# Performance work log

Measured on AMD Instinct MI355X. Metric: run time of the kernel, lower is better.

## Reference

```python
import jax, jax.numpy as jnp
import numpy as np

BN_EPS = 1e-5

def _ste_sign(x):
    # forward: sign in {-1,+1}; backward: clipped straight-through (grad 1 on [-1,1])
    s = jnp.where(x >= 0, 1.0, -1.0).astype(x.dtype)
    c = jnp.clip(x, -1.0, 1.0)
    return c + jax.lax.stop_gradient(s - c)

def setup_inputs() -> dict:
    key = jax.random.key(0)
    ks = jax.random.split(key, 8)
    N, C, H, W = 32, 256, 56, 56
    x = jax.random.normal(ks[0], (N, C, H, W), dtype=jnp.float32)
    bias0 = jax.random.normal(ks[1], (C,), dtype=jnp.float32) * 0.1
    w = jax.random.normal(ks[2], (C, C, 1, 1), dtype=jnp.float32) * 0.05
    gamma = jnp.ones((C,), dtype=jnp.float32)
    beta = jnp.zeros((C,), dtype=jnp.float32)
    bias1 = jax.random.normal(ks[3], (C,), dtype=jnp.float32) * 0.1
    alpha = jnp.full((C,), 0.25, dtype=jnp.float32)  # PReLU init
    bias2 = jax.random.normal(ks[4], (C,), dtype=jnp.float32) * 0.1
    return {"x": x, "bias0": bias0, "w": w, "gamma": gamma, "beta": beta,
            "bias1": bias1, "alpha": alpha, "bias2": bias2}

def reference(x, bias0, w, gamma, beta, bias1, alpha, bias2):
    ch = lambda v: v[None, :, None, None]
    # move0: learnable per-channel bias
    out = x + ch(bias0)
    # binary activation: sign (STE)
    out = _ste_sign(out)
    # binarized 1x1 conv: w_bin = mean(|w|) per out-channel * sign(w)
    scale = jnp.mean(jnp.abs(w), axis=(1, 2, 3))              # [O]
    wb = scale[:, None] * _ste_sign(w[:, :, 0, 0])            # [O, C]
    out = jnp.einsum('nchw,oc->nohw', out, wb)                # 1x1 conv
    # bn1: batch statistics (training-mode math)
    mu = jnp.mean(out, axis=(0, 2, 3), keepdims=True)
    var = jnp.var(out, axis=(0, 2, 3), keepdims=True)
    out = ch(gamma) * (out - mu) * jax.lax.rsqrt(var + BN_EPS) + ch(beta)
    # residual add (downsample is None)
    out = out + x
    # move1 -> PReLU -> move2
    out = out + ch(bias1)
    out = jnp.where(out > 0, out, ch(alpha) * out)
    out = out + ch(bias2)
    return out
```

## Files before the change

kernel.cpp:

```cpp
#include <hip/hip_runtime.h>
#include <stdint.h>

typedef unsigned long long u64;
typedef unsigned int u32;

constexpr int kC  = 256;
constexpr int kHW = 3136;
constexpr int kN  = 32;
constexpr int kP  = kN * kHW;
constexpr int kPos = 64;
constexpr int kBlk = kP / kPos;
constexpr int kRedBlk  = 16;
constexpr int kRedRows = kBlk / kRedBlk;

constexpr size_t OFF_T     = 0;
constexpr size_t OFF_SCALE = 8192;
constexpr size_t OFF_SUMD  = 9216;
constexpr size_t OFF_SUMD2 = 11264;
constexpr size_t OFF_S     = 13312;
constexpr size_t OFF_PS    = 3224576;
constexpr size_t OFF_PQ    = 4830208;

struct alignas(16) U64x2 { u64 x, y; };

__global__ __launch_bounds__(256) void prep_kernel(
    const float* __restrict__ w, char* __restrict__ ws) {
  int t = threadIdx.x;
  int b = blockIdx.x;
  u64*   T     = (u64*)(ws + OFF_T);
  float* scale = (float*)(ws + OFF_SCALE);
  int kk = t >> 6, ln = t & 63;
  if (b == 0) {
    ((u64*)(ws + OFF_SUMD))[t]  = 0ull;
    ((u64*)(ws + OFF_SUMD2))[t] = 0ull;
  }
  __shared__ float part[4][16];
#pragma unroll
  for (int i = 0; i < 16; ++i) {
    int o = b * 16 + i;
    float v = w[o * kC + kk * 64 + ln];
    u64 m = __ballot(v >= 0.0f);
    float a = fabsf(v);
#pragma unroll
    for (int s = 32; s > 0; s >>= 1) a += __shfl_xor(a, s, 64);
    if (ln == 0) { T[kk * 256 + o] = m; part[kk][i] = a; }
  }
  __syncthreads();
  if (t < 16) {
    int o = b * 16 + t;
    scale[o] = (part[0][t] + part[1][t] + part[2][t] + part[3][t]) * (1.0f / 256.0f);
  }
}

__global__ __launch_bounds__(256) void pack_stats_kernel(
    const float* __restrict__ x, const float* __restrict__ bias0,
    char* __restrict__ ws) {
  int t = threadIdx.x;
  int b = blockIdx.x;
  int k    = __builtin_amdgcn_readfirstlane(t >> 6);
  int lane = t & 63;
  u32 pb = (u32)b * (u32)kPos;
  u32 p  = pb + (u32)lane;
  u32 n  = p / kHW;
  u32 hw = p - n * kHW;
  const float* xp = x + (size_t)n * kC * kHW + (size_t)(k * 64) * kHW + hw;
  const float* bp = bias0 + k * 64;

  u64 m = 0;
#pragma unroll 32
  for (int i = 0; i < 64; ++i) {
    float v = xp[(size_t)i * kHW] + bp[i];
    m |= (u64)(v >= 0.0f) << i;
  }
  u64* S = (u64*)(ws + OFF_S);
  S[(size_t)k * kP + p] = m;

  __syncthreads();

  const u64* T = (const u64*)(ws + OFF_T);
  u64 t0 = T[t], t1 = T[256 + t], t2 = T[512 + t], t3 = T[768 + t];
  int summ = 0, summ2 = 0;
#pragma unroll 8
  for (int j = 0; j < kPos; j += 2) {
    u32 q = pb + j;
    U64x2 a0 = *(const U64x2*)&S[q];
    U64x2 a1 = *(const U64x2*)&S[kP + q];
    U64x2 a2 = *(const U64x2*)&S[2 * kP + q];
    U64x2 a3 = *(const U64x2*)&S[3 * kP + q];
    int ka = __popcll(a0.x ^ t0) + __popcll(a1.x ^ t1) +
             __popcll(a2.x ^ t2) + __popcll(a3.x ^ t3);
    int kb = __popcll(a0.y ^ t0) + __popcll(a1.y ^ t1) +
             __popcll(a2.y ^ t2) + __popcll(a3.y ^ t3);
    int ma = 128 - ka, mb = 128 - kb;
    summ  += ma + mb;
    summ2 += ma * ma + mb * mb;
  }
  ((int*)(ws + OFF_PS))[b * 256 + t] = summ;
  ((int*)(ws + OFF_PQ))[b * 256 + t] = summ2;
}

__global__ __launch_bounds__(256) void reduce_kernel(char* __restrict__ ws) {
  int t = threadIdx.x;
  int b = blockIdx.x;
  const int* PS = (const int*)(ws + OFF_PS);
  const int* PQ = (const int*)(ws + OFF_PQ);
  long long s = 0, q = 0;
#pragma unroll 7
  for (int r = 0; r < kRedRows; ++r) {
    int row = b * kRedRows + r;
    s += PS[row * 256 + t];
    q += PQ[row * 256 + t];
  }
  atomicAdd((u64*)(ws + OFF_SUMD) + t,  (u64)(long long)(2 * s));
  atomicAdd((u64*)(ws + OFF_SUMD2) + t, (u64)(long long)(4 * q));
}

__global__ __launch_bounds__(256) void finalize_kernel(
    const float* __restrict__ x, const float* __restrict__ gamma,
    const float* __restrict__ beta, const float* __restrict__ bias1,
    const float* __restrict__ alpha, const float* __restrict__ bias2,
    const char* __restrict__ ws, float* __restrict__ out) {
  __shared__ u64    ldsT[256][4];
  __shared__ float4 ldsC[256];

  int t = threadIdx.x;
  {
    const u64* T = (const u64*)(ws + OFF_T);
#pragma unroll
    for (int q = 0; q < 4; ++q) ldsT[t][q] = T[q * 256 + t];

    const float*     scale = (const float*)(ws + OFF_SCALE);
    const long long* sumd  = (const long long*)(ws + OFF_SUMD);
    const long long* sumd2 = (const long long*)(ws + OFF_SUMD2);
    double inv  = 1.0 / (double)kP;
    double md   = (double)sumd[t] * inv;
    double e2   = (double)sumd2[t] * inv;
    double vard = e2 - md * md;
    float sc  = scale[t];
    float mu  = sc * (float)md;
    float var = sc * sc * (float)vard;
    float rs  = rsqrtf(var + 1e-5f);
    float g   = gamma[t];
    float cA  = g * rs * sc;
    float cB  = beta[t] - g * rs * mu + bias1[t];
    ldsC[t] = make_float4(2.0f * cA, cB, alpha[t], bias2[t]);
  }
  __syncthreads();

  int k    = __builtin_amdgcn_readfirstlane(t >> 6);
  int lane = t & 63;
  u32 p  = blockIdx.x * (u32)kPos + (u32)lane;
  u32 n  = p / kHW;
  u32 hw = p - n * kHW;

  const u64* S = (const u64*)(ws + OFF_S);
  u64 s0 = S[p];
  u64 s1 = S[kP + p];
  u64 s2 = S[2 * kP + p];
  u64 s3 = S[3 * kP + p];

  const float* xp = x   + (size_t)n * kC * kHW + (size_t)(k * 64) * kHW + hw;
  float*       op = out + (size_t)n * kC * kHW + (size_t)(k * 64) * kHW + hw;

#pragma unroll 8
  for (int i = 0; i < 64; ++i) {
    int o = k * 64 + i;
    u64 w0 = ldsT[o][0], w1 = ldsT[o][1], w2 = ldsT[o][2], w3 = ldsT[o][3];
    int kx = __popcll(s0 ^ w0) + __popcll(s1 ^ w1) +
             __popcll(s2 ^ w2) + __popcll(s3 ^ w3);
    float4 cc = ldsC[o];
    float xv = xp[(size_t)i * kHW];
    float u  = fmaf(cc.x, (float)(128 - kx), cc.y) + xv;
    float r  = u > 0.0f ? u : cc.z * u;
    __builtin_nontemporal_store(r + cc.w, op + (size_t)i * kHW);
  }
}

extern "C" void kernel_launch(void* const* d_in, const int* in_sizes, int n_in,
                              void* d_out, int out_size, void* d_ws, size_t ws_size,
                              hipStream_t stream) {
  const float* x     = (const float*)d_in[0];
  const float* bias0 = (const float*)d_in[1];
  const float* w     = (const float*)d_in[2];
  const float* gamma = (const float*)d_in[3];
  const float* beta  = (const float*)d_in[4];
  const float* bias1 = (const float*)d_in[5];
  const float* alpha = (const float*)d_in[6];
  const float* bias2 = (const float*)d_in[7];
  float* out = (float*)d_out;
  char*  ws  = (char*)d_ws;

  hipLaunchKernelGGL(prep_kernel, dim3(16), dim3(256), 0, stream, w, ws);
  hipLaunchKernelGGL(pack_stats_kernel, dim3(kBlk), dim3(256), 0, stream,
                     x, bias0, ws);
  hipLaunchKernelGGL(reduce_kernel, dim3(kRedBlk), dim3(256), 0, stream, ws);
  hipLaunchKernelGGL(finalize_kernel, dim3(kBlk), dim3(256), 0, stream,
                     x, gamma, beta, bias1, alpha, bias2, ws, out);
}
```

Baseline: 255.6 us.

## Vectorize pack/finalize to 4 positions per lane and split stats into LDS-tiled kernel

```diff
diff --git a/kernel.cpp b/kernel.cpp
--- a/kernel.cpp
+++ b/kernel.cpp
@@ -3,15 +3,16 @@
 
 typedef unsigned long long u64;
 typedef unsigned int u32;
+typedef float f32x4 __attribute__((ext_vector_type(4)));
 
 constexpr int kC  = 256;
 constexpr int kHW = 3136;
 constexpr int kN  = 32;
 constexpr int kP  = kN * kHW;
-constexpr int kPos = 64;
-constexpr int kBlk = kP / kPos;
-constexpr int kRedBlk  = 16;
-constexpr int kRedRows = kBlk / kRedBlk;
+constexpr int kTile = 256;
+constexpr int kBlkT = kP / kTile;
+constexpr int kRedBlk  = 8;
+constexpr int kRedRows = kBlkT / kRedBlk;
 
 constexpr size_t OFF_T     = 0;
 constexpr size_t OFF_SCALE = 8192;
@@ -52,51 +53,58 @@
   }
 }
 
-__global__ __launch_bounds__(256) void pack_stats_kernel(
+__global__ __launch_bounds__(256) void pack_kernel(
     const float* __restrict__ x, const float* __restrict__ bias0,
     char* __restrict__ ws) {
   int t = threadIdx.x;
-  int b = blockIdx.x;
   int k    = __builtin_amdgcn_readfirstlane(t >> 6);
   int lane = t & 63;
-  u32 pb = (u32)b * (u32)kPos;
-  u32 p  = pb + (u32)lane;
-  u32 n  = p / kHW;
-  u32 hw = p - n * kHW;
-  const float* xp = x + (size_t)n * kC * kHW + (size_t)(k * 64) * kHW + hw;
+  u32 p0 = (u32)blockIdx.x * (u32)kTile + 4u * (u32)lane;
+  u32 n  = p0 / kHW;
+  u32 hw = p0 - n * kHW;
+  const float* xp = x + (size_t)(n * kC + k * 64) * kHW + hw;
   const float* bp = bias0 + k * 64;
 
-  u64 m = 0;
-#pragma unroll 32
+  u64 m0 = 0, m1 = 0, m2 = 0, m3 = 0;
+#pragma unroll 8
   for (int i = 0; i < 64; ++i) {
-    float v = xp[(size_t)i * kHW] + bp[i];
-    m |= (u64)(v >= 0.0f) << i;
-  }
-  u64* S = (u64*)(ws + OFF_S);
-  S[(size_t)k * kP + p] = m;
-
-  __syncthreads();
+    f32x4 v = *(const f32x4*)(xp + (size_t)i * kHW);
+    float bc = bp[i];
+    m0 |= (u64)(v.x + bc >= 0.0f) << i;
+    m1 |= (u64)(v.y + bc >= 0.0f) << i;
+    m2 |= (u64)(v.z + bc >= 0.0f) << i;
+    m3 |= (u64)(v.w + bc >= 0.0f) << i;
+  }
+  u64* Sp = (u64*)(ws + OFF_S) + (size_t)k * kP + p0;
+  U64x2 a; a.x = m0; a.y = m1;
+  U64x2 b; b.x = m2; b.y = m3;
+  *(U64x2*)Sp       = a;
+  *(U64x2*)(Sp + 2) = b;
+}
+
+__global__ __launch_bounds__(256) void stats_kernel(char* __restrict__ ws) {
+  __shared__ u64 tile[4][kTile];
+  int t = threadIdx.x;
+  u32 pb = blockIdx.x * (u32)kTile;
+  const u64* S = (const u64*)(ws + OFF_S);
+#pragma unroll
+  for (int q = 0; q < 4; ++q) tile[q][t] = S[(size_t)q * kP + pb + t];
 
   const u64* T = (const u64*)(ws + OFF_T);
   u64 t0 = T[t], t1 = T[256 + t], t2 = T[512 + t], t3 = T[768 + t];
+  __syncthreads();
+
   int summ = 0, summ2 = 0;
-#pragma unroll 8
-  for (int j = 0; j < kPos; j += 2) {
-    u32 q = pb + j;
-    U64x2 a0 = *(const U64x2*)&S[q];
-    U64x2 a1 = *(const U64x2*)&S[kP + q];
-    U64x2 a2 = *(const U64x2*)&S[2 * kP + q];
-    U64x2 a3 = *(const U64x2*)&S[3 * kP + q];
-    int ka = __popcll(a0.x ^ t0) + __popcll(a1.x ^ t1) +
-             __popcll(a2.x ^ t2) + __popcll(a3.x ^ t3);
-    int kb = __popcll(a0.y ^ t0) + __popcll(a1.y ^ t1) +
-             __popcll(a2.y ^ t2) + __popcll(a3.y ^ t3);
-    int ma = 128 - ka, mb = 128 - kb;
-    summ  += ma + mb;
-    summ2 += ma * ma + mb * mb;
-  }
-  ((int*)(ws + OFF_PS))[b * 256 + t] = summ;
-  ((int*)(ws + OFF_PQ))[b * 256 + t] = summ2;
+#pragma unroll 4
+  for (int j = 0; j < kTile; ++j) {
+    int kx = __popcll(tile[0][j] ^ t0) + __popcll(tile[1][j] ^ t1) +
+             __popcll(tile[2][j] ^ t2) + __popcll(tile[3][j] ^ t3);
+    int mm = 128 - kx;
+    summ  += mm;
+    summ2 += mm * mm;
+  }
+  ((int*)(ws + OFF_PS))[blockIdx.x * 256 + t] = summ;
+  ((int*)(ws + OFF_PQ))[blockIdx.x * 256 + t] = summ2;
 }
 
 __global__ __launch_bounds__(256) void reduce_kernel(char* __restrict__ ws) {
@@ -120,8 +128,8 @@
     const float* __restrict__ beta, const float* __restrict__ bias1,
     const float* __restrict__ alpha, const float* __restrict__ bias2,
     const char* __restrict__ ws, float* __restrict__ out) {
-  __shared__ u64    ldsT[256][4];
-  __shared__ float4 ldsC[256];
+  __shared__ u64   ldsT[256][4];
+  __shared__ f32x4 ldsC[256];
 
   int t = threadIdx.x;
   {
@@ -143,36 +151,50 @@
     float g   = gamma[t];
     float cA  = g * rs * sc;
     float cB  = beta[t] - g * rs * mu + bias1[t];
-    ldsC[t] = make_float4(2.0f * cA, cB, alpha[t], bias2[t]);
+    f32x4 cc; cc.x = 2.0f * cA; cc.y = cB; cc.z = alpha[t]; cc.w = bias2[t];
+    ldsC[t] = cc;
   }
   __syncthreads();
 
   int k    = __builtin_amdgcn_readfirstlane(t >> 6);
   int lane = t & 63;
-  u32 p  = blockIdx.x * (u32)kPos + (u32)lane;
-  u32 n  = p / kHW;
-  u32 hw = p - n * kHW;
+  u32 p0 = (u32)blockIdx.x * (u32)kTile + 4u * (u32)lane;
+  u32 n  = p0 / kHW;
+  u32 hw = p0 - n * kHW;
 
   const u64* S = (const u64*)(ws + OFF_S);
-  u64 s0 = S[p];
-  u64 s1 = S[kP + p];
-  u64 s2 = S[2 * kP + p];
-  u64 s3 = S[3 * kP + p];
-
-  const float* xp = x   + (size_t)n * kC * kHW + (size_t)(k * 64) * kHW + hw;
-  float*       op = out + (size_t)n * kC * kHW + (size_t)(k * 64) * kHW + hw;
-
-#pragma unroll 8
+  U64x2 a0 = *(const U64x2*)&S[p0],          b0 = *(const U64x2*)&S[p0 + 2];
+  U64x2 a1 = *(const U64x2*)&S[kP + p0],     b1 = *(const U64x2*)&S[kP + p0 + 2];
+  U64x2 a2 = *(const U64x2*)&S[2 * kP + p0], b2 = *(const U64x2*)&S[2 * kP + p0 + 2];
+  U64x2 a3 = *(const U64x2*)&S[3 * kP + p0], b3 = *(const U64x2*)&S[3 * kP + p0 + 2];
+
+  const float* xp = x   + (size_t)(n * kC + k * 64) * kHW + hw;
+  float*       op = out + (size_t)(n * kC + k * 64) * kHW + hw;
+
+#pragma unroll 4
   for (int i = 0; i < 64; ++i) {
     int o = k * 64 + i;
     u64 w0 = ldsT[o][0], w1 = ldsT[o][1], w2 = ldsT[o][2], w3 = ldsT[o][3];
-    int kx = __popcll(s0 ^ w0) + __popcll(s1 ^ w1) +
-             __popcll(s2 ^ w2) + __popcll(s3 ^ w3);
-    float4 cc = ldsC[o];
-    float xv = xp[(size_t)i * kHW];
-    float u  = fmaf(cc.x, (float)(128 - kx), cc.y) + xv;
-    float r  = u > 0.0f ? u : cc.z * u;
-    __builtin_nontemporal_store(r + cc.w, op + (size_t)i * kHW);
+    f32x4 cc = ldsC[o];
+    f32x4 xv = *(const f32x4*)(xp + (size_t)i * kHW);
+    int k0 = __popcll(a0.x ^ w0) + __popcll(a1.x ^ w1) +
+             __popcll(a2.x ^ w2) + __popcll(a3.x ^ w3);
+    int k1 = __popcll(a0.y ^ w0) + __popcll(a1.y ^ w1) +
+             __popcll(a2.y ^ w2) + __popcll(a3.y ^ w3);
+    int k2 = __popcll(b0.x ^ w0) + __popcll(b1.x ^ w1) +
+             __popcll(b2.x ^ w2) + __popcll(b3.x ^ w3);
+    int k3 = __popcll(b0.y ^ w0) + __popcll(b1.y ^ w1) +
+             __popcll(b2.y ^ w2) + __popcll(b3.y ^ w3);
+    float u0 = fmaf(cc.x, (float)(128 - k0), cc.y) + xv.x;
+    float u1 = fmaf(cc.x, (float)(128 - k1), cc.y) + xv.y;
+    float u2 = fmaf(cc.x, (float)(128 - k2), cc.y) + xv.z;
+    float u3 = fmaf(cc.x, (float)(128 - k3), cc.y) + xv.w;
+    f32x4 r;
+    r.x = (u0 > 0.0f ? u0 : cc.z * u0) + cc.w;
+    r.y = (u1 > 0.0f ? u1 : cc.z * u1) + cc.w;
+    r.z = (u2 > 0.0f ? u2 : cc.z * u2) + cc.w;
+    r.w = (u3 > 0.0f ? u3 : cc.z * u3) + cc.w;
+    __builtin_nontemporal_store(r, (f32x4*)(op + (size_t)i * kHW));
   }
 }
 
@@ -191,9 +213,10 @@
   char*  ws  = (char*)d_ws;
 
   hipLaunchKernelGGL(prep_kernel, dim3(16), dim3(256), 0, stream, w, ws);
-  hipLaunchKernelGGL(pack_stats_kernel, dim3(kBlk), dim3(256), 0, stream,
+  hipLaunchKernelGGL(pack_kernel, dim3(kBlkT), dim3(256), 0, stream,
                      x, bias0, ws);
+  hipLaunchKernelGGL(stats_kernel, dim3(kBlkT), dim3(256), 0, stream, ws);
   hipLaunchKernelGGL(reduce_kernel, dim3(kRedBlk), dim3(256), 0, stream, ws);
-  hipLaunchKernelGGL(finalize_kernel, dim3(kBlk), dim3(256), 0, stream,
+  hipLaunchKernelGGL(finalize_kernel, dim3(kBlkT), dim3(256), 0, stream,
                      x, gamma, beta, bias1, alpha, bias2, ws, out);
 }
```

Result: no change. 255.7 us (+0.0%).

## Fuse stats reduction into pack kernel with LDS tile and direct atomics

Applied to the files above, without the earlier changes.

```diff
diff --git a/kernel.cpp b/kernel.cpp
--- a/kernel.cpp
+++ b/kernel.cpp
@@ -3,23 +3,22 @@
 
 typedef unsigned long long u64;
 typedef unsigned int u32;
+typedef float f32x2 __attribute__((ext_vector_type(2)));
 
 constexpr int kC  = 256;
 constexpr int kHW = 3136;
 constexpr int kN  = 32;
 constexpr int kP  = kN * kHW;
-constexpr int kPos = 64;
-constexpr int kBlk = kP / kPos;
-constexpr int kRedBlk  = 16;
-constexpr int kRedRows = kBlk / kRedBlk;
+constexpr int kPosPk = 128;
+constexpr int kBlkPk = kP / kPosPk;
+constexpr int kPosFn = 64;
+constexpr int kBlkFn = kP / kPosFn;
 
 constexpr size_t OFF_T     = 0;
 constexpr size_t OFF_SCALE = 8192;
 constexpr size_t OFF_SUMD  = 9216;
 constexpr size_t OFF_SUMD2 = 11264;
 constexpr size_t OFF_S     = 13312;
-constexpr size_t OFF_PS    = 3224576;
-constexpr size_t OFF_PQ    = 4830208;
 
 struct alignas(16) U64x2 { u64 x, y; };
 
@@ -55,64 +54,46 @@
 __global__ __launch_bounds__(256) void pack_stats_kernel(
     const float* __restrict__ x, const float* __restrict__ bias0,
     char* __restrict__ ws) {
+  __shared__ U64x2 tile[4][64];
   int t = threadIdx.x;
-  int b = blockIdx.x;
   int k    = __builtin_amdgcn_readfirstlane(t >> 6);
   int lane = t & 63;
-  u32 pb = (u32)b * (u32)kPos;
-  u32 p  = pb + (u32)lane;
-  u32 n  = p / kHW;
-  u32 hw = p - n * kHW;
-  const float* xp = x + (size_t)n * kC * kHW + (size_t)(k * 64) * kHW + hw;
+  u32 pb = (u32)blockIdx.x * (u32)kPosPk;
+  u32 p0 = pb + 2u * (u32)lane;
+  u32 n  = p0 / kHW;
+  u32 hw = p0 - n * kHW;
+  const float* xp = x + (size_t)(n * kC + k * 64) * kHW + hw;
   const float* bp = bias0 + k * 64;
 
-  u64 m = 0;
-#pragma unroll 32
+  u64 m0 = 0, m1 = 0;
+#pragma unroll 8
   for (int i = 0; i < 64; ++i) {
-    float v = xp[(size_t)i * kHW] + bp[i];
-    m |= (u64)(v >= 0.0f) << i;
+    f32x2 v = *(const f32x2*)(xp + (size_t)i * kHW);
+    float bc = bp[i];
+    m0 |= (u64)(v.x + bc >= 0.0f) << i;
+    m1 |= (u64)(v.y + bc >= 0.0f) << i;
   }
-  u64* S = (u64*)(ws + OFF_S);
-  S[(size_t)k * kP + p] = m;
-
+  U64x2 mm; mm.x = m0; mm.y = m1;
+  tile[k][lane] = mm;
+  *(U64x2*)((u64*)(ws + OFF_S) + (size_t)k * kP + p0) = mm;
   __syncthreads();
 
   const u64* T = (const u64*)(ws + OFF_T);
   u64 t0 = T[t], t1 = T[256 + t], t2 = T[512 + t], t3 = T[768 + t];
-  int summ = 0, summ2 = 0;
+  int s = 0, sq = 0;
 #pragma unroll 8
-  for (int j = 0; j < kPos; j += 2) {
-    u32 q = pb + j;
-    U64x2 a0 = *(const U64x2*)&S[q];
-    U64x2 a1 = *(const U64x2*)&S[kP + q];
-    U64x2 a2 = *(const U64x2*)&S[2 * kP + q];
-    U64x2 a3 = *(const U64x2*)&S[3 * kP + q];
+  for (int j = 0; j < 64; ++j) {
+    U64x2 a0 = tile[0][j], a1 = tile[1][j], a2 = tile[2][j], a3 = tile[3][j];
     int ka = __popcll(a0.x ^ t0) + __popcll(a1.x ^ t1) +
              __popcll(a2.x ^ t2) + __popcll(a3.x ^ t3);
     int kb = __popcll(a0.y ^ t0) + __popcll(a1.y ^ t1) +
              __popcll(a2.y ^ t2) + __popcll(a3.y ^ t3);
     int ma = 128 - ka, mb = 128 - kb;
-    summ  += ma + mb;
-    summ2 += ma * ma + mb * mb;
-  }
-  ((int*)(ws + OFF_PS))[b * 256 + t] = summ;
-  ((int*)(ws + OFF_PQ))[b * 256 + t] = summ2;
-}
-
-__global__ __launch_bounds__(256) void reduce_kernel(char* __restrict__ ws) {
-  int t = threadIdx.x;
-  int b = blockIdx.x;
-  const int* PS = (const int*)(ws + OFF_PS);
-  const int* PQ = (const int*)(ws + OFF_PQ);
-  long long s = 0, q = 0;
-#pragma unroll 7
-  for (int r = 0; r < kRedRows; ++r) {
-    int row = b * kRedRows + r;
-    s += PS[row * 256 + t];
-    q += PQ[row * 256 + t];
+    s  += ma + mb;
+    sq += ma * ma + mb * mb;
   }
   atomicAdd((u64*)(ws + OFF_SUMD) + t,  (u64)(long long)(2 * s));
-  atomicAdd((u64*)(ws + OFF_SUMD2) + t, (u64)(long long)(4 * q));
+  atomicAdd((u64*)(ws + OFF_SUMD2) + t, (u64)(long long)(4 * sq));
 }
 
 __global__ __launch_bounds__(256) void finalize_kernel(
@@ -149,7 +130,7 @@
 
   int k    = __builtin_amdgcn_readfirstlane(t >> 6);
   int lane = t & 63;
-  u32 p  = blockIdx.x * (u32)kPos + (u32)lane;
+  u32 p  = blockIdx.x * (u32)kPosFn + (u32)lane;
   u32 n  = p / kHW;
   u32 hw = p - n * kHW;
 
@@ -159,8 +140,8 @@
   u64 s2 = S[2 * kP + p];
   u64 s3 = S[3 * kP + p];
 
-  const float* xp = x   + (size_t)n * kC * kHW + (size_t)(k * 64) * kHW + hw;
-  float*       op = out + (size_t)n * kC * kHW + (size_t)(k * 64) * kHW + hw;
+  const float* xp = x   + (size_t)(n * kC + k * 64) * kHW + hw;
+  float*       op = out + (size_t)(n * kC + k * 64) * kHW + hw;
 
 #pragma unroll 8
   for (int i = 0; i < 64; ++i) {
@@ -191,9 +172,8 @@
   char*  ws  = (char*)d_ws;
 
   hipLaunchKernelGGL(prep_kernel, dim3(16), dim3(256), 0, stream, w, ws);
-  hipLaunchKernelGGL(pack_stats_kernel, dim3(kBlk), dim3(256), 0, stream,
+  hipLaunchKernelGGL(pack_stats_kernel, dim3(kBlkPk), dim3(256), 0, stream,
                      x, bias0, ws);
-  hipLaunchKernelGGL(reduce_kernel, dim3(kRedBlk), dim3(256), 0, stream, ws);
-  hipLaunchKernelGGL(finalize_kernel, dim3(kBlk), dim3(256), 0, stream,
+  hipLaunchKernelGGL(finalize_kernel, dim3(kBlkFn), dim3(256), 0, stream,
                      x, gamma, beta, bias1, alpha, bias2, ws, out);
 }
```

After: 244.7 us. 1.04x faster.
